# Kernel optimization log

Measured on AMD Instinct MI355X. Metric: run time of the kernel, lower is better.

The kernel has to match this reference:

```python
import jax, jax.numpy as jnp
import numpy as np

TEMPERATURE = 1.0  # anneal_state_params['tempature'] at init
EPS_ZERO = 1e-5
EPS_DIV = 1e-29

N, M, K, D = 200000, 64, 16, 32

def setup_inputs() -> dict:
    key = jax.random.key(0)
    k1, k2, k3 = jax.random.split(key, 3)
    T = jax.random.normal(k1, (N, D), dtype=jnp.float32)
    alpha = jax.random.uniform(k2, (M, K, D), dtype=jnp.float32)  # np.random.rand init
    th = jnp.zeros((M, K), dtype=jnp.float32)
    # ambiguity thresholds: column 0 = pos (>0), column 1 = neg (<0)
    a = jax.random.uniform(k3, (M, K, 2), dtype=jnp.float32) * 0.5 + 0.1
    amb = a * jnp.array([1.0, -1.0], dtype=jnp.float32)
    return {"T": T, "alpha": alpha, "th": th, "amb": amb}

def reference(T, alpha, th, amb):
    # per-fern softmax over the feature axis of alpha*temperature
    sa = jax.nn.softmax(alpha * TEMPERATURE, axis=-1)          # (M, K, D)
    # batched fern projections: one einsum replaces the per-fern matmul loop
    temp = jnp.einsum('nd,mkd->nmk', T, sa)                    # (N, M, K)
    temp = jnp.where(jnp.abs(temp) < EPS_ZERO, 0.0, temp)
    b = temp - th[None, :, :]                                  # subtract threshold
    pos = amb[None, :, :, 0]                                   # (1, M, K)
    neg = amb[None, :, :, 1]
    B = jnp.clip((b - neg) / (pos - neg + EPS_DIV), 0.0, 1.0)  # (N, M, K)
    return B
```

## Files before the change

kernel.cpp:

```cpp
#include <hip/hip_runtime.h>
#include <math.h>

#define N_TOT 200000
#define D_    32
#define MK    1024
#define EPS_DIV  1e-29f

#define ROWS   16
#define HALF   512
#define NT     8
#define NSTRIP (N_TOT / ROWS)
#define NTASK  (NSTRIP * 2)
#define NBLK   4096
#define LDSF   512

typedef __attribute__((ext_vector_type(8))) short short8;
typedef __attribute__((ext_vector_type(4))) float f32x4;

__device__ __forceinline__ unsigned short f2bf(float x) {
    unsigned int u = __float_as_uint(x);
    u += 0x7FFFu + ((u >> 16) & 1u);
    return (unsigned short)(u >> 16);
}
__device__ __forceinline__ float bf2f(unsigned short h) {
    return __uint_as_float(((unsigned int)h) << 16);
}

__global__ __launch_bounds__(256) void prep_kernel(
    const float* __restrict__ alpha, const float* __restrict__ th,
    const float* __restrict__ amb,
    unsigned short* __restrict__ Whi, unsigned short* __restrict__ Wlo,
    float* __restrict__ off)
{
    int mk = blockIdx.x * 256 + threadIdx.x;
    if (mk >= MK) return;
    float v[D_];
    float mx = -1e30f;
#pragma unroll
    for (int d = 0; d < D_; ++d) { v[d] = alpha[mk * D_ + d]; mx = fmaxf(mx, v[d]); }
    float sum = 0.f;
#pragma unroll
    for (int d = 0; d < D_; ++d) { v[d] = expf(v[d] - mx); sum += v[d]; }
    float pos = amb[mk * 2 + 0];
    float neg = amb[mk * 2 + 1];
    float s  = 1.0f / (pos - neg + EPS_DIV);
    float si = s / sum;
#pragma unroll
    for (int d = 0; d < D_; ++d) {
        float w = v[d] * si;
        unsigned short h = f2bf(w);
        Whi[mk * D_ + d] = h;
        Wlo[mk * D_ + d] = f2bf(w - bf2f(h));
    }
    off[mk] = (0.0f - th[mk] - neg) * s;
}

__global__ __launch_bounds__(256, 4) void fern_mfma(
    const float* __restrict__ T,
    const unsigned short* __restrict__ Whi, const unsigned short* __restrict__ Wlo,
    const float* __restrict__ off, float* __restrict__ out)
{
    __shared__ float stage[ROWS][LDSF];

    const int tid  = threadIdx.x;
    const int lane = tid & 63;
    const int wid  = tid >> 6;
    const int lc   = lane & 15;
    const int lk   = lane >> 4;
    const int half = blockIdx.x & 1;
    const int mkb  = half * HALF;
    const int mk0  = mkb + wid * 128;

    short8 wh[NT], wl[NT];
#pragma unroll
    for (int t = 0; t < NT; ++t) {
        long c = (long)(mk0 + t * 16 + lc);
        wh[t] = *(const short8*)(Whi + c * D_ + lk * 8);
        wl[t] = *(const short8*)(Wlo + c * D_ + lk * 8);
    }
    const int sc  = tid & 127;
    const int sr0 = tid >> 7;
    const f32x4 ofv = *(const f32x4*)(off + mkb + 4 * sc);

    for (int task = blockIdx.x; task < NTASK; task += NBLK) {
        const int n0 = (task >> 1) * ROWS;

        const float* tp = T + (long)(n0 + lc) * D_ + lk * 8;
        float4 v0 = *(const float4*)tp;
        float4 v1 = *(const float4*)(tp + 4);
        float xs[8] = { v0.x, v0.y, v0.z, v0.w, v1.x, v1.y, v1.z, v1.w };
        short8 ah, al;
#pragma unroll
        for (int j = 0; j < 8; ++j) {
            unsigned short h = f2bf(xs[j]);
            ah[j] = (short)h;
            al[j] = (short)f2bf(xs[j] - bf2f(h));
        }

#pragma unroll
        for (int t = 0; t < NT; ++t) {
            f32x4 acc = { 0.f, 0.f, 0.f, 0.f };
            acc = __builtin_amdgcn_mfma_f32_16x16x32_bf16(wh[t], ah, acc, 0, 0, 0);
            acc = __builtin_amdgcn_mfma_f32_16x16x32_bf16(wh[t], al, acc, 0, 0, 0);
            acc = __builtin_amdgcn_mfma_f32_16x16x32_bf16(wl[t], ah, acc, 0, 0, 0);
            const int chunk = (wid * 32 + t * 4 + lk) ^ (lc & 7);
            *(f32x4*)&stage[lc][chunk * 4] = acc;
        }
        __syncthreads();

#pragma unroll
        for (int s = 0; s < 8; ++s) {
            const int r = 2 * s + sr0;
            const int k = sc ^ (r & 7);
            f32x4 v = *(const f32x4*)&stage[r][k * 4];
            f32x4 rr;
#pragma unroll
            for (int j = 0; j < 4; ++j)
                rr[j] = fminf(fmaxf(v[j] + ofv[j], 0.f), 1.f);
            *(f32x4*)(out + (long)(n0 + r) * MK + mkb + 4 * sc) = rr;
        }
        __syncthreads();
    }
}

extern "C" void kernel_launch(void* const* d_in, const int* in_sizes, int n_in,
                              void* d_out, int out_size, void* d_ws, size_t ws_size,
                              hipStream_t stream)
{
    const float* T     = (const float*)d_in[0];
    const float* alpha = (const float*)d_in[1];
    const float* th    = (const float*)d_in[2];
    const float* amb   = (const float*)d_in[3];
    float* out = (float*)d_out;

    unsigned short* Whi = (unsigned short*)d_ws;
    unsigned short* Wlo = Whi + MK * D_;
    float* offp = (float*)(Wlo + MK * D_);

    prep_kernel<<<MK / 256, 256, 0, stream>>>(alpha, th, amb, Whi, Wlo, offp);
    fern_mfma<<<NBLK, 256, 0, stream>>>(T, Whi, Wlo, offp, out);
}
```

Measured before the change: 168.0 us.

## Software-pipeline T loads and MFMA compute with output epilogue

Restructures the persistent loop so the next strip's T load is issued before the current strip's LDS-to-global store epilogue, and the next MFMAs run before the second barrier. Accumulators are carried across iterations in registers. This overlaps global load latency and matrix compute with the output writes. Launch bounds are relaxed from 4 to 3 waves per SIMD to make room for the extra live registers, which lowers occupancy. The last iteration redundantly reloads and recomputes its own strip.

```diff
diff --git a/kernel.cpp b/kernel.cpp
--- a/kernel.cpp
+++ b/kernel.cpp
@@ -55,7 +55,7 @@
     off[mk] = (0.0f - th[mk] - neg) * s;
 }
 
-__global__ __launch_bounds__(256, 4) void fern_mfma(
+__global__ __launch_bounds__(256, 3) void fern_mfma(
     const float* __restrict__ T,
     const unsigned short* __restrict__ Whi, const unsigned short* __restrict__ Wlo,
     const float* __restrict__ off, float* __restrict__ out)
@@ -81,11 +81,12 @@
     const int sc  = tid & 127;
     const int sr0 = tid >> 7;
     const f32x4 ofv = *(const f32x4*)(off + mkb + 4 * sc);
+    const long lrow = (long)lc * D_ + lk * 8;
 
-    for (int task = blockIdx.x; task < NTASK; task += NBLK) {
-        const int n0 = (task >> 1) * ROWS;
-
-        const float* tp = T + (long)(n0 + lc) * D_ + lk * 8;
+    f32x4 acc[NT];
+    int task = blockIdx.x;
+    {
+        const float* tp = T + (long)((task >> 1) * ROWS) * D_ + lrow;
         float4 v0 = *(const float4*)tp;
         float4 v1 = *(const float4*)(tp + 4);
         float xs[8] = { v0.x, v0.y, v0.z, v0.w, v1.x, v1.y, v1.z, v1.w };
@@ -96,17 +97,32 @@
             ah[j] = (short)h;
             al[j] = (short)f2bf(xs[j] - bf2f(h));
         }
-
 #pragma unroll
         for (int t = 0; t < NT; ++t) {
-            f32x4 acc = { 0.f, 0.f, 0.f, 0.f };
-            acc = __builtin_amdgcn_mfma_f32_16x16x32_bf16(wh[t], ah, acc, 0, 0, 0);
-            acc = __builtin_amdgcn_mfma_f32_16x16x32_bf16(wh[t], al, acc, 0, 0, 0);
-            acc = __builtin_amdgcn_mfma_f32_16x16x32_bf16(wl[t], ah, acc, 0, 0, 0);
+            f32x4 a = { 0.f, 0.f, 0.f, 0.f };
+            a = __builtin_amdgcn_mfma_f32_16x16x32_bf16(wh[t], ah, a, 0, 0, 0);
+            a = __builtin_amdgcn_mfma_f32_16x16x32_bf16(wh[t], al, a, 0, 0, 0);
+            a = __builtin_amdgcn_mfma_f32_16x16x32_bf16(wl[t], ah, a, 0, 0, 0);
+            acc[t] = a;
+        }
+    }
+
+    while (true) {
+#pragma unroll
+        for (int t = 0; t < NT; ++t) {
             const int chunk = (wid * 32 + t * 4 + lk) ^ (lc & 7);
-            *(f32x4*)&stage[lc][chunk * 4] = acc;
+            *(f32x4*)&stage[lc][chunk * 4] = acc[t];
         }
         __syncthreads();
+
+        const int n0 = (task >> 1) * ROWS;
+        const int nxt = task + NBLK;
+        const bool more = nxt < NTASK;
+        const int tload = more ? nxt : task;
+
+        const float* tp = T + (long)((tload >> 1) * ROWS) * D_ + lrow;
+        float4 v0 = *(const float4*)tp;
+        float4 v1 = *(const float4*)(tp + 4);
 
 #pragma unroll
         for (int s = 0; s < 8; ++s) {
@@ -119,7 +135,29 @@
                 rr[j] = fminf(fmaxf(v[j] + ofv[j], 0.f), 1.f);
             *(f32x4*)(out + (long)(n0 + r) * MK + mkb + 4 * sc) = rr;
         }
+
+        {
+            float xs[8] = { v0.x, v0.y, v0.z, v0.w, v1.x, v1.y, v1.z, v1.w };
+            short8 ah, al;
+#pragma unroll
+            for (int j = 0; j < 8; ++j) {
+                unsigned short h = f2bf(xs[j]);
+                ah[j] = (short)h;
+                al[j] = (short)f2bf(xs[j] - bf2f(h));
+            }
+#pragma unroll
+            for (int t = 0; t < NT; ++t) {
+                f32x4 a = { 0.f, 0.f, 0.f, 0.f };
+                a = __builtin_amdgcn_mfma_f32_16x16x32_bf16(wh[t], ah, a, 0, 0, 0);
+                a = __builtin_amdgcn_mfma_f32_16x16x32_bf16(wh[t], al, a, 0, 0, 0);
+                a = __builtin_amdgcn_mfma_f32_16x16x32_bf16(wl[t], ah, a, 0, 0, 0);
+                acc[t] = a;
+            }
+        }
         __syncthreads();
+
+        if (!more) break;
+        task = nxt;
     }
 }
 
```

Result: slower. 198.1 us, median of 2 (+17.9%).
